# Performance work log

Measured on AMD Instinct MI355X. Metric: run time of the kernel, lower is better.

## Reference

```python
import jax, jax.numpy as jnp
import numpy as np

QBITS = 8  # fake-quant bit width from q_config
DT_RANK = 128
D_STATE = 16


def fake_quant_tensor(x, bits=QBITS):
    """Per-tensor symmetric fake quantization (quantize-dequantize) with STE."""
    qmax = 2.0 ** (bits - 1) - 1.0
    s = jnp.maximum(jnp.max(jnp.abs(x)) / qmax, 1e-8)
    q = jnp.clip(jnp.round(x / s), -qmax - 1.0, qmax) * s
    return x + jax.lax.stop_gradient(q - x)


def fake_quant_per_channel(w, bits=QBITS):
    """Per-output-channel symmetric fake quantization for weights [out, in]."""
    qmax = 2.0 ** (bits - 1) - 1.0
    s = jnp.maximum(jnp.max(jnp.abs(w), axis=-1, keepdims=True) / qmax, 1e-8)
    q = jnp.clip(jnp.round(w / s), -qmax - 1.0, qmax) * s
    return w + jax.lax.stop_gradient(q - w)


def setup_inputs() -> dict:
    key = jax.random.key(0)
    ks = jax.random.split(key, 8)
    B, L, D_MODEL = 2, 4096, 2048
    d_inner = D_MODEL  # expand = 1.0
    x = jax.random.normal(ks[0], (B, L, D_MODEL), jnp.float32)
    prompt = 0.1 * jax.random.normal(ks[1], (B, L, D_STATE), jnp.float32)
    # x_proj: Linear(d_inner -> dt_rank + 2*d_state), no bias
    Wx = jax.random.normal(ks[2], (DT_RANK + 2 * D_STATE, d_inner), jnp.float32) / np.sqrt(d_inner)
    # dt_proj: Linear(dt_rank -> d_inner), with bias
    Wdt = jax.random.normal(ks[3], (d_inner, DT_RANK), jnp.float32) / np.sqrt(DT_RANK)
    bdt = 0.1 * jax.random.normal(ks[4], (d_inner,), jnp.float32)
    # S4D-real init for A_log, D skip param (standard Mamba selective-scan params)
    A_log = jnp.log(jnp.tile(jnp.arange(1, D_STATE + 1, dtype=jnp.float32), (d_inner, 1)))
    Dskip = jax.random.normal(ks[5], (d_inner,), jnp.float32)
    return dict(x=x, prompt=prompt, Wx=Wx, Wdt=Wdt, bdt=bdt, A_log=A_log, Dskip=Dskip)


def reference(x, prompt, Wx, Wdt, bdt, A_log, Dskip):
    # x_proj with fake-quantized weight, then split into dt / B / C
    x_dbl = jnp.einsum('bld,od->blo', x, fake_quant_per_channel(Wx))
    dts = x_dbl[..., :DT_RANK]
    Bs = x_dbl[..., DT_RANK:DT_RANK + D_STATE]
    Cs = x_dbl[..., DT_RANK + D_STATE:]
    # dt_proj with fake-quantized weight
    dts = jnp.einsum('blr,or->blo', dts, fake_quant_per_channel(Wdt)) + bdt
    # activation fake-quant of scan inputs
    u_q = fake_quant_tensor(x)          # [B, L, d_inner]
    dt_q = fake_quant_tensor(dts)       # [B, L, d_inner]
    B_q = fake_quant_tensor(Bs)         # [B, L, d_state]
    C_q = fake_quant_tensor(Cs + prompt)  # [B, L, d_state]
    # selective scan (quantized SSM weights A, D)
    A = -jnp.exp(fake_quant_per_channel(A_log))  # [d_inner, d_state]
    D_q = fake_quant_tensor(Dskip)               # [d_inner]
    dt = jax.nn.softplus(dt_q)

    def step(h, inp):
        u_t, dt_t, B_t, C_t = inp  # [B,d], [B,d], [B,n], [B,n]
        dA = jnp.exp(dt_t[:, :, None] * A)             # [B, d, n]
        dBu = (dt_t * u_t)[:, :, None] * B_t[:, None, :]
        h = dA * h + dBu                               # [B, d, n]
        y = jnp.einsum('bdn,bn->bd', h, C_t)
        return h, y

    Bsz, L, d = x.shape
    h0 = jnp.zeros((Bsz, d, D_STATE), x.dtype)
    xs = (jnp.swapaxes(u_q, 0, 1), jnp.swapaxes(dt, 0, 1),
          jnp.swapaxes(B_q, 0, 1), jnp.swapaxes(C_q, 0, 1))
    _, ys = jax.lax.scan(step, h0, xs)  # ys: [L, B, d]
    return jnp.swapaxes(ys, 0, 1) + u_q * D_q
```

## Files before the change

kernel.cpp:

```cpp
#include <hip/hip_runtime.h>
#include <hip/hip_bf16.h>

#define BSZ    2
#define LSEQ   4096
#define DMODEL 2048
#define DTR    128
#define DST    16
#define ODIM   160
#define MROWS  (BSZ*LSEQ)
#define CH     64
#define TT     (LSEQ/CH)
#define LOG2E  1.44269504088896340736f
#define LN2    0.69314718055994530942f

typedef short  short8  __attribute__((ext_vector_type(8)));
typedef float  floatx4 __attribute__((ext_vector_type(4)));

__device__ __forceinline__ unsigned short f2bf(float f) {
    unsigned u = __float_as_uint(f);
    u += 0x7fffu + ((u >> 16) & 1u);
    return (unsigned short)(u >> 16);
}
__device__ __forceinline__ float quantv(float x, float s, float inv_s) {
    float q = rintf(x * inv_s);
    q = fminf(fmaxf(q, -128.0f), 127.0f);
    return q * s;
}
__device__ __forceinline__ float softplus_fast(float v) {
    float t = __builtin_amdgcn_exp2f(-fabsf(v) * LOG2E);
    return fmaxf(v, 0.0f) + LN2 * __log2f(1.0f + t);
}
__device__ __forceinline__ float scale_from_bits(unsigned bits) {
    return fmaxf(__uint_as_float(bits) * (1.0f/127.0f), 1e-8f);
}
__device__ __forceinline__ int pidx(int r, int k, int K) {
    return (r >> 4)*(16*K) + ((k >> 5) << 9) + (((r & 15) + (((k & 31) >> 3) << 4)) << 3) + (k & 7);
}

#define PB_WX  160
#define PB_WDT 128
#define PB_A   128
#define PB_D   1
#define PREP_BLOCKS (PB_WX + PB_WDT + PB_A + PB_D)

__global__ __launch_bounds__(256) void k_prep(
    const float* __restrict__ Wx, const float* __restrict__ Wdt,
    const float* __restrict__ A_log, const float* __restrict__ Dskip,
    unsigned short* __restrict__ Wxq, unsigned short* __restrict__ Wdtq,
    float* __restrict__ a2, float* __restrict__ Dq)
{
    int bid = blockIdx.x, tid = threadIdx.x;
    __shared__ float red[256];
    if (bid < PB_WX) {
        int o = bid, base = o * DMODEL;
        float m = 0.0f;
        for (int i = tid; i < DMODEL; i += 256) m = fmaxf(m, fabsf(Wx[base+i]));
        red[tid] = m; __syncthreads();
        for (int s2 = 128; s2 > 0; s2 >>= 1) { if (tid < s2) red[tid] = fmaxf(red[tid], red[tid+s2]); __syncthreads(); }
        float s = fmaxf(red[0]*(1.0f/127.0f), 1e-8f), inv = 1.0f/s;
        for (int i = tid; i < DMODEL; i += 256)
            Wxq[pidx(o, i, DMODEL)] = f2bf(quantv(Wx[base+i], s, inv));
    } else if (bid < PB_WX + PB_WDT) {
        int n = (bid - PB_WX)*16 + (tid >> 4);
        int k0 = (tid & 15)*8;
        const float* src = Wdt + (size_t)n*DTR + k0;
        float4 v0 = *reinterpret_cast<const float4*>(src);
        float4 v1 = *reinterpret_cast<const float4*>(src + 4);
        float m = fmaxf(fmaxf(fmaxf(fabsf(v0.x), fabsf(v0.y)), fmaxf(fabsf(v0.z), fabsf(v0.w))),
                        fmaxf(fmaxf(fabsf(v1.x), fabsf(v1.y)), fmaxf(fabsf(v1.z), fabsf(v1.w))));
        for (int off = 1; off < 16; off <<= 1) m = fmaxf(m, __shfl_xor(m, off, 16));
        float s = fmaxf(m*(1.0f/127.0f), 1e-8f), inv = 1.0f/s;
        short8 o8;
        o8[0]=(short)f2bf(quantv(v0.x,s,inv)); o8[1]=(short)f2bf(quantv(v0.y,s,inv));
        o8[2]=(short)f2bf(quantv(v0.z,s,inv)); o8[3]=(short)f2bf(quantv(v0.w,s,inv));
        o8[4]=(short)f2bf(quantv(v1.x,s,inv)); o8[5]=(short)f2bf(quantv(v1.y,s,inv));
        o8[6]=(short)f2bf(quantv(v1.z,s,inv)); o8[7]=(short)f2bf(quantv(v1.w,s,inv));
        *reinterpret_cast<short8*>(Wdtq + pidx(n, k0, DTR)) = o8;
    } else if (bid < PB_WX + PB_WDT + PB_A) {
        int d = (bid - PB_WX - PB_WDT)*16 + (tid >> 4);
        int n = tid & 15;
        float v = A_log[d*DST + n];
        float m = fabsf(v);
        for (int off = 1; off < 16; off <<= 1) m = fmaxf(m, __shfl_xor(m, off, 16));
        float s = fmaxf(m*(1.0f/127.0f), 1e-8f);
        float q = quantv(v, s, 1.0f/s);
        a2[d*DST + n] = -expf(q) * LOG2E;
    } else {
        float m = 0.0f;
        for (int i = tid; i < DMODEL; i += 256) m = fmaxf(m, fabsf(Dskip[i]));
        red[tid] = m; __syncthreads();
        for (int s2 = 128; s2 > 0; s2 >>= 1) { if (tid < s2) red[tid] = fmaxf(red[tid], red[tid+s2]); __syncthreads(); }
        float s = fmaxf(red[0]*(1.0f/127.0f), 1e-8f), inv = 1.0f/s;
        for (int i = tid; i < DMODEL; i += 256) Dq[i] = quantv(Dskip[i], s, inv);
    }
}

__global__ __launch_bounds__(256) void k_mm1(
    const float* __restrict__ x, const unsigned short* __restrict__ Wxq,
    const float* __restrict__ prompt,
    unsigned short* __restrict__ xdblbf, float* __restrict__ xbc,
    unsigned* __restrict__ scales)
{
    int tid = threadIdx.x, w = tid >> 6, lane = tid & 63;
    int mrow = lane & 15, quad = lane >> 4;
    int mt = blockIdx.x, m0 = mt*16, k0 = w*512;
    floatx4 acc[10] = {};
    float xmax = 0.0f;
    const float* arow = x + (size_t)(m0 + mrow)*DMODEL + k0 + quad*8;
    for (int kk = 0; kk < 512; kk += 32) {
        const float4* ap = reinterpret_cast<const float4*>(arow + kk);
        float4 a0 = ap[0], a1 = ap[1];
        xmax = fmaxf(xmax, fmaxf(fmaxf(fabsf(a0.x), fabsf(a0.y)), fmaxf(fabsf(a0.z), fabsf(a0.w))));
        xmax = fmaxf(xmax, fmaxf(fmaxf(fabsf(a1.x), fabsf(a1.y)), fmaxf(fabsf(a1.z), fabsf(a1.w))));
        short8 af;
        af[0]=(short)f2bf(a0.x); af[1]=(short)f2bf(a0.y); af[2]=(short)f2bf(a0.z); af[3]=(short)f2bf(a0.w);
        af[4]=(short)f2bf(a1.x); af[5]=(short)f2bf(a1.y); af[6]=(short)f2bf(a1.z); af[7]=(short)f2bf(a1.w);
        int kcidx = (k0 + kk) >> 5;
        #pragma unroll
        for (int j = 0; j < 10; ++j) {
            short8 bf = *reinterpret_cast<const short8*>(Wxq + j*16*DMODEL + kcidx*512 + lane*8);
            acc[j] = __builtin_amdgcn_mfma_f32_16x16x32_bf16(af, bf, acc[j], 0, 0, 0);
        }
    }
    for (int off = 32; off; off >>= 1) xmax = fmaxf(xmax, __shfl_xor(xmax, off, 64));
    __shared__ float red[4*2560];
    __shared__ float redB[256], redC[256];
    __shared__ float wred[4];
    if (lane == 0) wred[w] = xmax;
    #pragma unroll
    for (int j = 0; j < 10; ++j) {
        float4 v = make_float4(acc[j][0], acc[j][1], acc[j][2], acc[j][3]);
        *reinterpret_cast<float4*>(&red[w*2560 + (j*16 + mrow)*16 + quad*4]) = v;
    }
    __syncthreads();
    float bmax = 0.0f, cmax = 0.0f;
    #pragma unroll
    for (int j = 0; j < 10; ++j) {
        int e = j*256 + tid;
        float v = red[e] + red[2560+e] + red[5120+e] + red[7680+e];
        int col = e >> 4, rowin = e & 15, row = m0 + rowin;
        if (col < DTR) {
            xdblbf[mt*16*DTR + ((col>>5)<<9) + ((rowin + (((col&31)>>3)<<4))<<3) + (col&7)] = f2bf(v);
        } else if (col < DTR + DST) {
            bmax = fmaxf(bmax, fabsf(v));
            xbc[(size_t)row*32 + (col - DTR)] = v;
        } else {
            v += prompt[(size_t)row*DST + (col - DTR - DST)];
            cmax = fmaxf(cmax, fabsf(v));
            xbc[(size_t)row*32 + 16 + (col - DTR - DST)] = v;
        }
    }
    redB[tid] = bmax; redC[tid] = cmax; __syncthreads();
    for (int s2 = 128; s2 > 0; s2 >>= 1) {
        if (tid < s2) { redB[tid] = fmaxf(redB[tid], redB[tid+s2]); redC[tid] = fmaxf(redC[tid], redC[tid+s2]); }
        __syncthreads();
    }
    if (tid == 0) {
        atomicMax(&scales[0], __float_as_uint(fmaxf(fmaxf(wred[0], wred[1]), fmaxf(wred[2], wred[3]))));
        atomicMax(&scales[1], __float_as_uint(redB[0]));
        atomicMax(&scales[2], __float_as_uint(redC[0]));
    }
}

__global__ __launch_bounds__(256) void k_dmaxu(
    const unsigned short* __restrict__ Ap, const unsigned short* __restrict__ Bp,
    const float* __restrict__ bdt, const float* __restrict__ x,
    signed char* __restrict__ u8, unsigned* __restrict__ scales)
{
    int tid = threadIdx.x, w = tid >> 6, lane = tid & 63;
    int mrow = lane & 15;
    int mt = blockIdx.x >> 4, nt = blockIdx.x & 15;
    int mtile = mt*4 + w, n0 = nt*128;
    short8 afr[4];
    const unsigned short* ab = Ap + (size_t)mtile*16*DTR + lane*8;
    #pragma unroll
    for (int kc = 0; kc < 4; ++kc) afr[kc] = *reinterpret_cast<const short8*>(ab + (kc<<9));
    float dmax = 0.0f;
    #pragma unroll
    for (int j = 0; j < 8; ++j) {
        const unsigned short* bb = Bp + (size_t)(n0/16 + j)*16*DTR + lane*8;
        floatx4 acc = {};
        #pragma unroll
        for (int kc = 0; kc < 4; ++kc) {
            short8 bf = *reinterpret_cast<const short8*>(bb + (kc<<9));
            acc = __builtin_amdgcn_mfma_f32_16x16x32_bf16(afr[kc], bf, acc, 0, 0, 0);
        }
        float bv = bdt[n0 + j*16 + mrow];
        #pragma unroll
        for (int r = 0; r < 4; ++r) dmax = fmaxf(dmax, fabsf(acc[r] + bv));
    }
    float s_u = scale_from_bits(scales[0]);
    float inv_su = 1.0f / s_u;
    const float4* xs = reinterpret_cast<const float4*>(x) + (size_t)blockIdx.x*2048;
    unsigned* uo = reinterpret_cast<unsigned*>(u8) + (size_t)blockIdx.x*2048;
    #pragma unroll
    for (int i = 0; i < 8; ++i) {
        float4 v = xs[i*256 + tid];
        int q0 = (int)fminf(fmaxf(rintf(v.x*inv_su), -128.0f), 127.0f);
        int q1 = (int)fminf(fmaxf(rintf(v.y*inv_su), -128.0f), 127.0f);
        int q2 = (int)fminf(fmaxf(rintf(v.z*inv_su), -128.0f), 127.0f);
        int q3 = (int)fminf(fmaxf(rintf(v.w*inv_su), -128.0f), 127.0f);
        uo[i*256 + tid] = (q0 & 255) | ((q1 & 255) << 8) | ((q2 & 255) << 16) | ((unsigned)(q3 & 255) << 24);
    }
    for (int off = 32; off; off >>= 1) dmax = fmaxf(dmax, __shfl_xor(dmax, off, 64));
    __shared__ float wd[4];
    if (lane == 0) wd[w] = dmax;
    __syncthreads();
    if (tid == 0)
        atomicMax(&scales[3], __float_as_uint(fmaxf(fmaxf(wd[0], wd[1]), fmaxf(wd[2], wd[3]))));
}

__global__ __launch_bounds__(256) void k_scan1(
    const unsigned short* __restrict__ Ap, const unsigned short* __restrict__ Bp,
    const float* __restrict__ bdt, const signed char* __restrict__ u8,
    const float* __restrict__ xbc, const float* __restrict__ a2,
    const unsigned* __restrict__ scales,
    float* __restrict__ Aprod, float* __restrict__ hfin)
{
    int bid = blockIdx.x, tid = threadIdx.x;
    int w = tid >> 6, lane = tid & 63;
    int mrow = lane & 15, quad = lane >> 4;
    int b = bid >> 9, rem = bid & 511, dblk = rem >> 6, ch = rem & 63;
    int d0 = dblk*256, t0 = ch*TT;
    int d = d0 + tid;
    float s_u  = scale_from_bits(scales[0]);
    float s_B  = scale_from_bits(scales[1]), inv_sB  = 1.0f/s_B;
    float s_dt = scale_from_bits(scales[3]), inv_sdt = 1.0f/s_dt;
    float a2r[16];
    {
        const float4* ap = reinterpret_cast<const float4*>(a2 + (size_t)d*DST);
        float4 v0 = ap[0], v1 = ap[1], v2 = ap[2], v3 = ap[3];
        a2r[0]=v0.x; a2r[1]=v0.y; a2r[2]=v0.z; a2r[3]=v0.w;
        a2r[4]=v1.x; a2r[5]=v1.y; a2r[6]=v1.z; a2r[7]=v1.w;
        a2r[8]=v2.x; a2r[9]=v2.y; a2r[10]=v2.z; a2r[11]=v2.w;
        a2r[12]=v3.x; a2r[13]=v3.y; a2r[14]=v3.z; a2r[15]=v3.w;
    }
    float h[16];
    #pragma unroll
    for (int n = 0; n < 16; ++n) h[n] = 0.0f;
    float sdt = 0.0f;
    __shared__ float lds_dts[32*256];
    __shared__ unsigned lds_u[32*64];
    __shared__ __align__(16) float Bq_p[32*16];
    for (int st = 0; st < 2; ++st) {
        int tb = t0 + st*32;
        int gm0 = (b*LSEQ + tb) >> 4;
        short8 afr[2][4];
        #pragma unroll
        for (int rt = 0; rt < 2; ++rt)
            #pragma unroll
            for (int kc = 0; kc < 4; ++kc)
                afr[rt][kc] = *reinterpret_cast<const short8*>(Ap + (size_t)(gm0+rt)*16*DTR + (kc<<9) + lane*8);
        #pragma unroll
        for (int j = 0; j < 4; ++j) {
            int ntile = dblk*16 + w*4 + j;
            int dloc = w*64 + j*16 + mrow;
            float bdtv = bdt[d0 + dloc];
            short8 bfr[4];
            #pragma unroll
            for (int kc = 0; kc < 4; ++kc)
                bfr[kc] = *reinterpret_cast<const short8*>(Bp + (size_t)ntile*16*DTR + (kc<<9) + lane*8);
            #pragma unroll
            for (int rt = 0; rt < 2; ++rt) {
                floatx4 acc = {};
                #pragma unroll
                for (int kc = 0; kc < 4; ++kc)
                    acc = __builtin_amdgcn_mfma_f32_16x16x32_bf16(afr[rt][kc], bfr[kc], acc, 0, 0, 0);
                #pragma unroll
                for (int r = 0; r < 4; ++r)
                    lds_dts[(rt*16 + quad*4 + r)*256 + dloc] = acc[r] + bdtv;
            }
        }
        {
            const unsigned* ub = reinterpret_cast<const unsigned*>(u8 + (size_t)(b*LSEQ + tb)*DMODEL + d0);
            #pragma unroll
            for (int i = 0; i < 8; ++i) {
                int q = i*256 + tid;
                lds_u[q] = ub[(q >> 6)*(DMODEL/4) + (q & 63)];
            }
            int e = tid;
            Bq_p[e] = quantv(xbc[(size_t)(b*LSEQ + tb + (e>>4))*32 + (e&15)], s_B, inv_sB);
            e = tid + 256;
            Bq_p[e] = quantv(xbc[(size_t)(b*LSEQ + tb + (e>>4))*32 + (e&15)], s_B, inv_sB);
        }
        __syncthreads();
        const signed char* lub = reinterpret_cast<const signed char*>(lds_u);
        for (int t = 0; t < 32; ++t) {
            float dtq = quantv(lds_dts[t*256 + tid], s_dt, inv_sdt);
            float dtv = softplus_fast(dtq);
            float uq  = s_u * (float)lub[t*256 + tid];
            float dtu = dtv * uq;
            sdt += dtv;
            const float4* bq4 = reinterpret_cast<const float4*>(&Bq_p[t*16]);
            float4 b0 = bq4[0], b1 = bq4[1], b2 = bq4[2], b3 = bq4[3];
            float bq[16] = { b0.x,b0.y,b0.z,b0.w, b1.x,b1.y,b1.z,b1.w,
                             b2.x,b2.y,b2.z,b2.w, b3.x,b3.y,b3.z,b3.w };
            #pragma unroll
            for (int n = 0; n < 16; ++n) {
                float dA = __builtin_amdgcn_exp2f(a2r[n]*dtv);
                h[n] = fmaf(dA, h[n], dtu*bq[n]);
            }
        }
        __syncthreads();
    }
    size_t ob = ((size_t)((b*CH + ch)*DMODEL + d))*DST;
    #pragma unroll
    for (int i = 0; i < 4; ++i) {
        float4 av = make_float4(__builtin_amdgcn_exp2f(a2r[4*i+0]*sdt),
                                __builtin_amdgcn_exp2f(a2r[4*i+1]*sdt),
                                __builtin_amdgcn_exp2f(a2r[4*i+2]*sdt),
                                __builtin_amdgcn_exp2f(a2r[4*i+3]*sdt));
        float4 hv = make_float4(h[4*i+0], h[4*i+1], h[4*i+2], h[4*i+3]);
        *reinterpret_cast<float4*>(Aprod + ob + 4*i) = av;
        *reinterpret_cast<float4*>(hfin  + ob + 4*i) = hv;
    }
}

__global__ __launch_bounds__(256) void k_mid(
    float* __restrict__ Aprod, const float* __restrict__ hfin)
{
    int f = blockIdx.x*256 + threadIdx.x;
    int b = f >> 15, dn = f & 32767;
    size_t base = (size_t)b*CH*32768 + dn;
    float h = 0.0f;
    #pragma unroll 4
    for (int ch = 0; ch < CH; ++ch) {
        size_t o = base + (size_t)ch*32768;
        float a = Aprod[o], hf = hfin[o];
        Aprod[o] = h;
        h = fmaf(a, h, hf);
    }
}

__global__ __launch_bounds__(256) void k_scan3(
    const unsigned short* __restrict__ Ap, const unsigned short* __restrict__ Bp,
    const float* __restrict__ bdt, const signed char* __restrict__ u8,
    const float* __restrict__ xbc, const float* __restrict__ a2,
    const float* __restrict__ Dq, const unsigned* __restrict__ scales,
    const float* __restrict__ hinit, float* __restrict__ out)
{
    int bid = blockIdx.x, tid = threadIdx.x;
    int w = tid >> 6, lane = tid & 63;
    int mrow = lane & 15, quad = lane >> 4;
    int b = bid >> 9, rem = bid & 511, dblk = rem >> 6, ch = rem & 63;
    int d0 = dblk*256, t0 = ch*TT;
    int d = d0 + tid;
    float s_u  = scale_from_bits(scales[0]);
    float s_B  = scale_from_bits(scales[1]), inv_sB  = 1.0f/s_B;
    float s_C  = scale_from_bits(scales[2]), inv_sC  = 1.0f/s_C;
    float s_dt = scale_from_bits(scales[3]), inv_sdt = 1.0f/s_dt;
    float dqd = Dq[d];
    float a2r[16];
    {
        const float4* ap = reinterpret_cast<const float4*>(a2 + (size_t)d*DST);
        float4 v0 = ap[0], v1 = ap[1], v2 = ap[2], v3 = ap[3];
        a2r[0]=v0.x; a2r[1]=v0.y; a2r[2]=v0.z; a2r[3]=v0.w;
        a2r[4]=v1.x; a2r[5]=v1.y; a2r[6]=v1.z; a2r[7]=v1.w;
        a2r[8]=v2.x; a2r[9]=v2.y; a2r[10]=v2.z; a2r[11]=v2.w;
        a2r[12]=v3.x; a2r[13]=v3.y; a2r[14]=v3.z; a2r[15]=v3.w;
    }
    size_t ob = ((size_t)((b*CH + ch)*DMODEL + d))*DST;
    float h[16];
    #pragma unroll
    for (int i = 0; i < 4; ++i) {
        float4 hv = *reinterpret_cast<const float4*>(hinit + ob + 4*i);
        h[4*i+0]=hv.x; h[4*i+1]=hv.y; h[4*i+2]=hv.z; h[4*i+3]=hv.w;
    }
    __shared__ float lds_dts[32*256];
    __shared__ unsigned lds_u[32*64];
    __shared__ __align__(16) float Bq_p[32*16];
    __shared__ __align__(16) float Cq_p[32*16];
    for (int st = 0; st < 2; ++st) {
        int tb = t0 + st*32;
        int gm0 = (b*LSEQ + tb) >> 4;
        short8 afr[2][4];
        #pragma unroll
        for (int rt = 0; rt < 2; ++rt)
            #pragma unroll
            for (int kc = 0; kc < 4; ++kc)
                afr[rt][kc] = *reinterpret_cast<const short8*>(Ap + (size_t)(gm0+rt)*16*DTR + (kc<<9) + lane*8);
        #pragma unroll
        for (int j = 0; j < 4; ++j) {
            int ntile = dblk*16 + w*4 + j;
            int dloc = w*64 + j*16 + mrow;
            float bdtv = bdt[d0 + dloc];
            short8 bfr[4];
            #pragma unroll
            for (int kc = 0; kc < 4; ++kc)
                bfr[kc] = *reinterpret_cast<const short8*>(Bp + (size_t)ntile*16*DTR + (kc<<9) + lane*8);
            #pragma unroll
            for (int rt = 0; rt < 2; ++rt) {
                floatx4 acc = {};
                #pragma unroll
                for (int kc = 0; kc < 4; ++kc)
                    acc = __builtin_amdgcn_mfma_f32_16x16x32_bf16(afr[rt][kc], bfr[kc], acc, 0, 0, 0);
                #pragma unroll
                for (int r = 0; r < 4; ++r)
                    lds_dts[(rt*16 + quad*4 + r)*256 + dloc] = acc[r] + bdtv;
            }
        }
        {
            const unsigned* ub = reinterpret_cast<const unsigned*>(u8 + (size_t)(b*LSEQ + tb)*DMODEL + d0);
            #pragma unroll
            for (int i = 0; i < 8; ++i) {
                int q = i*256 + tid;
                lds_u[q] = ub[(q >> 6)*(DMODEL/4) + (q & 63)];
            }
            int e = tid;
            size_t px = (size_t)(b*LSEQ + tb + (e>>4))*32;
            Bq_p[e] = quantv(xbc[px + (e&15)],      s_B, inv_sB);
            Cq_p[e] = quantv(xbc[px + 16 + (e&15)], s_C, inv_sC);
            e = tid + 256;
            px = (size_t)(b*LSEQ + tb + (e>>4))*32;
            Bq_p[e] = quantv(xbc[px + (e&15)],      s_B, inv_sB);
            Cq_p[e] = quantv(xbc[px + 16 + (e&15)], s_C, inv_sC);
        }
        __syncthreads();
        const signed char* lub = reinterpret_cast<const signed char*>(lds_u);
        for (int t = 0; t < 32; ++t) {
            float dtq = quantv(lds_dts[t*256 + tid], s_dt, inv_sdt);
            float dtv = softplus_fast(dtq);
            float uq  = s_u * (float)lub[t*256 + tid];
            float dtu = dtv * uq;
            const float4* bq4 = reinterpret_cast<const float4*>(&Bq_p[t*16]);
            const float4* cq4 = reinterpret_cast<const float4*>(&Cq_p[t*16]);
            float4 b0 = bq4[0], b1 = bq4[1], b2 = bq4[2], b3 = bq4[3];
            float4 c0 = cq4[0], c1 = cq4[1], c2 = cq4[2], c3 = cq4[3];
            float bq[16] = { b0.x,b0.y,b0.z,b0.w, b1.x,b1.y,b1.z,b1.w,
                             b2.x,b2.y,b2.z,b2.w, b3.x,b3.y,b3.z,b3.w };
            float cq[16] = { c0.x,c0.y,c0.z,c0.w, c1.x,c1.y,c1.z,c1.w,
                             c2.x,c2.y,c2.z,c2.w, c3.x,c3.y,c3.z,c3.w };
            float y = 0.0f;
            #pragma unroll
            for (int n = 0; n < 16; ++n) {
                float dA = __builtin_amdgcn_exp2f(a2r[n]*dtv);
                h[n] = fmaf(dA, h[n], dtu*bq[n]);
                y = fmaf(h[n], cq[n], y);
            }
            __builtin_nontemporal_store(y + uq * dqd, out + (size_t)(b*LSEQ + tb + t)*DMODEL + d);
        }
        __syncthreads();
    }
}

extern "C" void kernel_launch(void* const* d_in, const int* in_sizes, int n_in,
                              void* d_out, int out_size, void* d_ws, size_t ws_size,
                              hipStream_t stream)
{
    const float* x      = (const float*)d_in[0];
    const float* prompt = (const float*)d_in[1];
    const float* Wx     = (const float*)d_in[2];
    const float* Wdt    = (const float*)d_in[3];
    const float* bdt    = (const float*)d_in[4];
    const float* A_log  = (const float*)d_in[5];
    const float* Dskip  = (const float*)d_in[6];
    float* out = (float*)d_out;
    char* ws = (char*)d_ws;
    size_t off = 0;
    unsigned* scales       = (unsigned*)(ws + off);        off += 256;
    unsigned short* Wxq    = (unsigned short*)(ws + off);  off += (size_t)ODIM*DMODEL*2;
    unsigned short* Wdtq   = (unsigned short*)(ws + off);  off += (size_t)DMODEL*DTR*2;
    float* a2              = (float*)(ws + off);           off += (size_t)DMODEL*DST*4;
    float* Dq              = (float*)(ws + off);           off += (size_t)DMODEL*4;
    float* xbc             = (float*)(ws + off);           off += (size_t)MROWS*32*4;
    unsigned short* xdblbf = (unsigned short*)(ws + off);  off += (size_t)MROWS*DTR*2;
    signed char* u8        = (signed char*)(ws + off);     off += (size_t)MROWS*DMODEL;
    float* Aprod           = (float*)(ws + off);           off += (size_t)BSZ*CH*DMODEL*DST*4;
    float* hfin            = (float*)(ws + off);           off += (size_t)BSZ*CH*DMODEL*DST*4;

    hipMemsetAsync(scales, 0, 256, stream);
    hipLaunchKernelGGL(k_prep, dim3(PREP_BLOCKS), dim3(256), 0, stream,
                       Wx, Wdt, A_log, Dskip, Wxq, Wdtq, a2, Dq);
    hipLaunchKernelGGL(k_mm1, dim3(MROWS/16), dim3(256), 0, stream,
                       x, Wxq, prompt, xdblbf, xbc, scales);
    hipLaunchKernelGGL(k_dmaxu, dim3((MROWS/64)*(DMODEL/128)), dim3(256), 0, stream,
                       xdblbf, Wdtq, bdt, x, u8, scales);
    hipLaunchKernelGGL(k_scan1, dim3(BSZ*8*CH), dim3(256), 0, stream,
                       xdblbf, Wdtq, bdt, u8, xbc, a2, scales, Aprod, hfin);
    hipLaunchKernelGGL(k_mid, dim3(BSZ*DMODEL*DST/256), dim3(256), 0, stream,
                       Aprod, hfin);
    hipLaunchKernelGGL(k_scan3, dim3(BSZ*8*CH), dim3(256), 0, stream,
                       xdblbf, Wdtq, bdt, u8, xbc, a2, Dq, scales, Aprod, out);
}
```

Baseline: 309.7 us.

## Fuse dt-max into x_proj kernel and u quantization into scan1, drop k_dmaxu

The dt_proj max-reduction moves into k_mm1, which now multiplies its 16-row tile by all of Wdt from LDS. The x-to-int8 quantization moves into k_scan1, which writes u8 for k_scan3. This removes a kernel launch and one pass that re-read x and the bf16 dt tiles. The scan kernels now stage 16 timesteps instead of 32, with a padded LDS stride, and pack the state update into two-wide float vectors that may map to packed FP32 instructions. In exchange, k_mm1 does much more MFMA and Wdt-load work per block, and the scan loops have more staging and barrier rounds.

```diff
diff --git a/kernel.cpp b/kernel.cpp
--- a/kernel.cpp
+++ b/kernel.cpp
@@ -10,11 +10,13 @@
 #define MROWS  (BSZ*LSEQ)
 #define CH     64
 #define TT     (LSEQ/CH)
+#define STRD   258
 #define LOG2E  1.44269504088896340736f
 #define LN2    0.69314718055994530942f
 
 typedef short  short8  __attribute__((ext_vector_type(8)));
 typedef float  floatx4 __attribute__((ext_vector_type(4)));
+typedef float  floatx2 __attribute__((ext_vector_type(2)));
 
 __device__ __forceinline__ unsigned short f2bf(float f) {
     unsigned u = __float_as_uint(f);
@@ -97,6 +99,7 @@
 
 __global__ __launch_bounds__(256) void k_mm1(
     const float* __restrict__ x, const unsigned short* __restrict__ Wxq,
+    const unsigned short* __restrict__ Wdtq, const float* __restrict__ bdt,
     const float* __restrict__ prompt,
     unsigned short* __restrict__ xdblbf, float* __restrict__ xbc,
     unsigned* __restrict__ scales)
@@ -125,7 +128,8 @@
     for (int off = 32; off; off >>= 1) xmax = fmaxf(xmax, __shfl_xor(xmax, off, 64));
     __shared__ float red[4*2560];
     __shared__ float redB[256], redC[256];
-    __shared__ float wred[4];
+    __shared__ float wred[4], wd[4];
+    __shared__ unsigned short lds_abf[2048];
     if (lane == 0) wred[w] = xmax;
     #pragma unroll
     for (int j = 0; j < 10; ++j) {
@@ -140,7 +144,10 @@
         float v = red[e] + red[2560+e] + red[5120+e] + red[7680+e];
         int col = e >> 4, rowin = e & 15, row = m0 + rowin;
         if (col < DTR) {
-            xdblbf[mt*16*DTR + ((col>>5)<<9) + ((rowin + (((col&31)>>3)<<4))<<3) + (col&7)] = f2bf(v);
+            int off = ((col>>5)<<9) + ((rowin + (((col&31)>>3)<<4))<<3) + (col&7);
+            unsigned short bfb = f2bf(v);
+            xdblbf[mt*16*DTR + off] = bfb;
+            lds_abf[off] = bfb;
         } else if (col < DTR + DST) {
             bmax = fmaxf(bmax, fabsf(v));
             xbc[(size_t)row*32 + (col - DTR)] = v;
@@ -155,66 +162,40 @@
         if (tid < s2) { redB[tid] = fmaxf(redB[tid], redB[tid+s2]); redC[tid] = fmaxf(redC[tid], redC[tid+s2]); }
         __syncthreads();
     }
+    short8 afr[4];
+    #pragma unroll
+    for (int kc = 0; kc < 4; ++kc)
+        afr[kc] = *reinterpret_cast<const short8*>(lds_abf + (kc<<9) + lane*8);
+    float dmax = 0.0f;
+    for (int jj = 0; jj < 32; ++jj) {
+        int ntile = w*32 + jj;
+        const unsigned short* bb = Wdtq + (size_t)ntile*16*DTR + lane*8;
+        floatx4 acc2 = {};
+        #pragma unroll
+        for (int kc = 0; kc < 4; ++kc) {
+            short8 bf = *reinterpret_cast<const short8*>(bb + (kc<<9));
+            acc2 = __builtin_amdgcn_mfma_f32_16x16x32_bf16(afr[kc], bf, acc2, 0, 0, 0);
+        }
+        float bv = bdt[ntile*16 + mrow];
+        #pragma unroll
+        for (int r = 0; r < 4; ++r) dmax = fmaxf(dmax, fabsf(acc2[r] + bv));
+    }
+    for (int off = 32; off; off >>= 1) dmax = fmaxf(dmax, __shfl_xor(dmax, off, 64));
+    if (lane == 0) wd[w] = dmax;
+    __syncthreads();
     if (tid == 0) {
         atomicMax(&scales[0], __float_as_uint(fmaxf(fmaxf(wred[0], wred[1]), fmaxf(wred[2], wred[3]))));
         atomicMax(&scales[1], __float_as_uint(redB[0]));
         atomicMax(&scales[2], __float_as_uint(redC[0]));
-    }
-}
-
-__global__ __launch_bounds__(256) void k_dmaxu(
+        atomicMax(&scales[3], __float_as_uint(fmaxf(fmaxf(wd[0], wd[1]), fmaxf(wd[2], wd[3]))));
+    }
+}
+
+__global__ __launch_bounds__(256) void k_scan1(
     const unsigned short* __restrict__ Ap, const unsigned short* __restrict__ Bp,
     const float* __restrict__ bdt, const float* __restrict__ x,
-    signed char* __restrict__ u8, unsigned* __restrict__ scales)
-{
-    int tid = threadIdx.x, w = tid >> 6, lane = tid & 63;
-    int mrow = lane & 15;
-    int mt = blockIdx.x >> 4, nt = blockIdx.x & 15;
-    int mtile = mt*4 + w, n0 = nt*128;
-    short8 afr[4];
-    const unsigned short* ab = Ap + (size_t)mtile*16*DTR + lane*8;
-    #pragma unroll
-    for (int kc = 0; kc < 4; ++kc) afr[kc] = *reinterpret_cast<const short8*>(ab + (kc<<9));
-    float dmax = 0.0f;
-    #pragma unroll
-    for (int j = 0; j < 8; ++j) {
-        const unsigned short* bb = Bp + (size_t)(n0/16 + j)*16*DTR + lane*8;
-        floatx4 acc = {};
-        #pragma unroll
-        for (int kc = 0; kc < 4; ++kc) {
-            short8 bf = *reinterpret_cast<const short8*>(bb + (kc<<9));
-            acc = __builtin_amdgcn_mfma_f32_16x16x32_bf16(afr[kc], bf, acc, 0, 0, 0);
-        }
-        float bv = bdt[n0 + j*16 + mrow];
-        #pragma unroll
-        for (int r = 0; r < 4; ++r) dmax = fmaxf(dmax, fabsf(acc[r] + bv));
-    }
-    float s_u = scale_from_bits(scales[0]);
-    float inv_su = 1.0f / s_u;
-    const float4* xs = reinterpret_cast<const float4*>(x) + (size_t)blockIdx.x*2048;
-    unsigned* uo = reinterpret_cast<unsigned*>(u8) + (size_t)blockIdx.x*2048;
-    #pragma unroll
-    for (int i = 0; i < 8; ++i) {
-        float4 v = xs[i*256 + tid];
-        int q0 = (int)fminf(fmaxf(rintf(v.x*inv_su), -128.0f), 127.0f);
-        int q1 = (int)fminf(fmaxf(rintf(v.y*inv_su), -128.0f), 127.0f);
-        int q2 = (int)fminf(fmaxf(rintf(v.z*inv_su), -128.0f), 127.0f);
-        int q3 = (int)fminf(fmaxf(rintf(v.w*inv_su), -128.0f), 127.0f);
-        uo[i*256 + tid] = (q0 & 255) | ((q1 & 255) << 8) | ((q2 & 255) << 16) | ((unsigned)(q3 & 255) << 24);
-    }
-    for (int off = 32; off; off >>= 1) dmax = fmaxf(dmax, __shfl_xor(dmax, off, 64));
-    __shared__ float wd[4];
-    if (lane == 0) wd[w] = dmax;
-    __syncthreads();
-    if (tid == 0)
-        atomicMax(&scales[3], __float_as_uint(fmaxf(fmaxf(wd[0], wd[1]), fmaxf(wd[2], wd[3]))));
-}
-
-__global__ __launch_bounds__(256) void k_scan1(
-    const unsigned short* __restrict__ Ap, const unsigned short* __restrict__ Bp,
-    const float* __restrict__ bdt, const signed char* __restrict__ u8,
     const float* __restrict__ xbc, const float* __restrict__ a2,
-    const unsigned* __restrict__ scales,
+    const unsigned* __restrict__ scales, unsigned* __restrict__ u8g,
     float* __restrict__ Aprod, float* __restrict__ hfin)
 {
     int bid = blockIdx.x, tid = threadIdx.x;
@@ -223,94 +204,88 @@
     int b = bid >> 9, rem = bid & 511, dblk = rem >> 6, ch = rem & 63;
     int d0 = dblk*256, t0 = ch*TT;
     int d = d0 + tid;
-    float s_u  = scale_from_bits(scales[0]);
+    float s_u  = scale_from_bits(scales[0]), inv_su = 1.0f/s_u;
     float s_B  = scale_from_bits(scales[1]), inv_sB  = 1.0f/s_B;
     float s_dt = scale_from_bits(scales[3]), inv_sdt = 1.0f/s_dt;
-    float a2r[16];
+    floatx2 a22[8];
     {
-        const float4* ap = reinterpret_cast<const float4*>(a2 + (size_t)d*DST);
-        float4 v0 = ap[0], v1 = ap[1], v2 = ap[2], v3 = ap[3];
-        a2r[0]=v0.x; a2r[1]=v0.y; a2r[2]=v0.z; a2r[3]=v0.w;
-        a2r[4]=v1.x; a2r[5]=v1.y; a2r[6]=v1.z; a2r[7]=v1.w;
-        a2r[8]=v2.x; a2r[9]=v2.y; a2r[10]=v2.z; a2r[11]=v2.w;
-        a2r[12]=v3.x; a2r[13]=v3.y; a2r[14]=v3.z; a2r[15]=v3.w;
-    }
-    float h[16];
-    #pragma unroll
-    for (int n = 0; n < 16; ++n) h[n] = 0.0f;
+        const floatx2* ap = reinterpret_cast<const floatx2*>(a2 + (size_t)d*DST);
+        #pragma unroll
+        for (int i = 0; i < 8; ++i) a22[i] = ap[i];
+    }
+    floatx2 h2[8];
+    #pragma unroll
+    for (int i = 0; i < 8; ++i) h2[i] = (floatx2){0.0f, 0.0f};
     float sdt = 0.0f;
-    __shared__ float lds_dts[32*256];
-    __shared__ unsigned lds_u[32*64];
-    __shared__ __align__(16) float Bq_p[32*16];
-    for (int st = 0; st < 2; ++st) {
-        int tb = t0 + st*32;
-        int gm0 = (b*LSEQ + tb) >> 4;
-        short8 afr[2][4];
-        #pragma unroll
-        for (int rt = 0; rt < 2; ++rt)
-            #pragma unroll
-            for (int kc = 0; kc < 4; ++kc)
-                afr[rt][kc] = *reinterpret_cast<const short8*>(Ap + (size_t)(gm0+rt)*16*DTR + (kc<<9) + lane*8);
+    __shared__ float lds_dts[16*STRD];
+    __shared__ unsigned lds_u[16*64];
+    __shared__ __align__(16) float Bq_p[16*16];
+    for (int st = 0; st < TT/16; ++st) {
+        int tb = t0 + st*16;
+        int gm = (b*LSEQ + tb) >> 4;
+        short8 afr[4];
+        #pragma unroll
+        for (int kc = 0; kc < 4; ++kc)
+            afr[kc] = *reinterpret_cast<const short8*>(Ap + (size_t)gm*16*DTR + (kc<<9) + lane*8);
         #pragma unroll
         for (int j = 0; j < 4; ++j) {
             int ntile = dblk*16 + w*4 + j;
             int dloc = w*64 + j*16 + mrow;
             float bdtv = bdt[d0 + dloc];
-            short8 bfr[4];
-            #pragma unroll
-            for (int kc = 0; kc < 4; ++kc)
-                bfr[kc] = *reinterpret_cast<const short8*>(Bp + (size_t)ntile*16*DTR + (kc<<9) + lane*8);
-            #pragma unroll
-            for (int rt = 0; rt < 2; ++rt) {
-                floatx4 acc = {};
-                #pragma unroll
-                for (int kc = 0; kc < 4; ++kc)
-                    acc = __builtin_amdgcn_mfma_f32_16x16x32_bf16(afr[rt][kc], bfr[kc], acc, 0, 0, 0);
-                #pragma unroll
-                for (int r = 0; r < 4; ++r)
-                    lds_dts[(rt*16 + quad*4 + r)*256 + dloc] = acc[r] + bdtv;
-            }
+            floatx4 acc = {};
+            #pragma unroll
+            for (int kc = 0; kc < 4; ++kc) {
+                short8 bf = *reinterpret_cast<const short8*>(Bp + (size_t)ntile*16*DTR + (kc<<9) + lane*8);
+                acc = __builtin_amdgcn_mfma_f32_16x16x32_bf16(afr[kc], bf, acc, 0, 0, 0);
+            }
+            #pragma unroll
+            for (int r = 0; r < 4; ++r)
+                lds_dts[(quad*4 + r)*STRD + dloc] = acc[r] + bdtv;
         }
         {
-            const unsigned* ub = reinterpret_cast<const unsigned*>(u8 + (size_t)(b*LSEQ + tb)*DMODEL + d0);
-            #pragma unroll
-            for (int i = 0; i < 8; ++i) {
-                int q = i*256 + tid;
-                lds_u[q] = ub[(q >> 6)*(DMODEL/4) + (q & 63)];
-            }
-            int e = tid;
-            Bq_p[e] = quantv(xbc[(size_t)(b*LSEQ + tb + (e>>4))*32 + (e&15)], s_B, inv_sB);
-            e = tid + 256;
-            Bq_p[e] = quantv(xbc[(size_t)(b*LSEQ + tb + (e>>4))*32 + (e&15)], s_B, inv_sB);
+            const float4* x4 = reinterpret_cast<const float4*>(x);
+            #pragma unroll
+            for (int i = 0; i < 4; ++i) {
+                int q = i*256 + tid, row = q >> 6, c4 = q & 63;
+                size_t gi = (size_t)(b*LSEQ + tb + row)*(DMODEL/4) + dblk*64 + c4;
+                float4 v = x4[gi];
+                int q0 = (int)fminf(fmaxf(rintf(v.x*inv_su), -128.0f), 127.0f);
+                int q1 = (int)fminf(fmaxf(rintf(v.y*inv_su), -128.0f), 127.0f);
+                int q2 = (int)fminf(fmaxf(rintf(v.z*inv_su), -128.0f), 127.0f);
+                int q3 = (int)fminf(fmaxf(rintf(v.w*inv_su), -128.0f), 127.0f);
+                unsigned u = (q0 & 255) | ((q1 & 255) << 8) | ((q2 & 255) << 16) | ((unsigned)(q3 & 255) << 24);
+                lds_u[row*64 + c4] = u;
+                u8g[gi] = u;
+            }
+            Bq_p[tid] = quantv(xbc[(size_t)(b*LSEQ + tb + (tid>>4))*32 + (tid&15)], s_B, inv_sB);
         }
         __syncthreads();
         const signed char* lub = reinterpret_cast<const signed char*>(lds_u);
-        for (int t = 0; t < 32; ++t) {
-            float dtq = quantv(lds_dts[t*256 + tid], s_dt, inv_sdt);
+        for (int t = 0; t < 16; ++t) {
+            float dtq = quantv(lds_dts[t*STRD + tid], s_dt, inv_sdt);
             float dtv = softplus_fast(dtq);
             float uq  = s_u * (float)lub[t*256 + tid];
             float dtu = dtv * uq;
             sdt += dtv;
-            const float4* bq4 = reinterpret_cast<const float4*>(&Bq_p[t*16]);
-            float4 b0 = bq4[0], b1 = bq4[1], b2 = bq4[2], b3 = bq4[3];
-            float bq[16] = { b0.x,b0.y,b0.z,b0.w, b1.x,b1.y,b1.z,b1.w,
-                             b2.x,b2.y,b2.z,b2.w, b3.x,b3.y,b3.z,b3.w };
-            #pragma unroll
-            for (int n = 0; n < 16; ++n) {
-                float dA = __builtin_amdgcn_exp2f(a2r[n]*dtv);
-                h[n] = fmaf(dA, h[n], dtu*bq[n]);
+            floatx2 dtv2 = {dtv, dtv}, dtu2 = {dtu, dtu};
+            const floatx2* bq2 = reinterpret_cast<const floatx2*>(&Bq_p[t*16]);
+            #pragma unroll
+            for (int n2 = 0; n2 < 8; ++n2) {
+                floatx2 e = a22[n2] * dtv2;
+                floatx2 dA; dA.x = __builtin_amdgcn_exp2f(e.x); dA.y = __builtin_amdgcn_exp2f(e.y);
+                h2[n2] = dA*h2[n2] + bq2[n2]*dtu2;
             }
         }
         __syncthreads();
     }
     size_t ob = ((size_t)((b*CH + ch)*DMODEL + d))*DST;
+    floatx2 sdt2 = {sdt, sdt};
     #pragma unroll
     for (int i = 0; i < 4; ++i) {
-        float4 av = make_float4(__builtin_amdgcn_exp2f(a2r[4*i+0]*sdt),
-                                __builtin_amdgcn_exp2f(a2r[4*i+1]*sdt),
-                                __builtin_amdgcn_exp2f(a2r[4*i+2]*sdt),
-                                __builtin_amdgcn_exp2f(a2r[4*i+3]*sdt));
-        float4 hv = make_float4(h[4*i+0], h[4*i+1], h[4*i+2], h[4*i+3]);
+        floatx2 e0 = a22[2*i] * sdt2, e1 = a22[2*i+1] * sdt2;
+        float4 av = make_float4(__builtin_amdgcn_exp2f(e0.x), __builtin_amdgcn_exp2f(e0.y),
+                                __builtin_amdgcn_exp2f(e1.x), __builtin_amdgcn_exp2f(e1.y));
+        float4 hv = make_float4(h2[2*i].x, h2[2*i].y, h2[2*i+1].x, h2[2*i+1].y);
         *reinterpret_cast<float4*>(Aprod + ob + 4*i) = av;
         *reinterpret_cast<float4*>(hfin  + ob + 4*i) = hv;
     }
@@ -334,7 +309,7 @@
 
 __global__ __launch_bounds__(256) void k_scan3(
     const unsigned short* __restrict__ Ap, const unsigned short* __restrict__ Bp,
-    const float* __restrict__ bdt, const signed char* __restrict__ u8,
+    const float* __restrict__ bdt, const unsigned* __restrict__ u8g,
     const float* __restrict__ xbc, const float* __restrict__ a2,
     const float* __restrict__ Dq, const unsigned* __restrict__ scales,
     const float* __restrict__ hinit, float* __restrict__ out)
@@ -350,93 +325,76 @@
     float s_C  = scale_from_bits(scales[2]), inv_sC  = 1.0f/s_C;
     float s_dt = scale_from_bits(scales[3]), inv_sdt = 1.0f/s_dt;
     float dqd = Dq[d];
-    float a2r[16];
+    floatx2 a22[8];
     {
-        const float4* ap = reinterpret_cast<const float4*>(a2 + (size_t)d*DST);
-        float4 v0 = ap[0], v1 = ap[1], v2 = ap[2], v3 = ap[3];
-        a2r[0]=v0.x; a2r[1]=v0.y; a2r[2]=v0.z; a2r[3]=v0.w;
-        a2r[4]=v1.x; a2r[5]=v1.y; a2r[6]=v1.z; a2r[7]=v1.w;
-        a2r[8]=v2.x; a2r[9]=v2.y; a2r[10]=v2.z; a2r[11]=v2.w;
-        a2r[12]=v3.x; a2r[13]=v3.y; a2r[14]=v3.z; a2r[15]=v3.w;
+        const floatx2* ap = reinterpret_cast<const floatx2*>(a2 + (size_t)d*DST);
+        #pragma unroll
+        for (int i = 0; i < 8; ++i) a22[i] = ap[i];
     }
     size_t ob = ((size_t)((b*CH + ch)*DMODEL + d))*DST;
-    float h[16];
+    floatx2 h2[8];
     #pragma unroll
     for (int i = 0; i < 4; ++i) {
         float4 hv = *reinterpret_cast<const float4*>(hinit + ob + 4*i);
-        h[4*i+0]=hv.x; h[4*i+1]=hv.y; h[4*i+2]=hv.z; h[4*i+3]=hv.w;
-    }
-    __shared__ float lds_dts[32*256];
-    __shared__ unsigned lds_u[32*64];
-    __shared__ __align__(16) float Bq_p[32*16];
-    __shared__ __align__(16) float Cq_p[32*16];
-    for (int st = 0; st < 2; ++st) {
-        int tb = t0 + st*32;
-        int gm0 = (b*LSEQ + tb) >> 4;
-        short8 afr[2][4];
-        #pragma unroll
-        for (int rt = 0; rt < 2; ++rt)
-            #pragma unroll
-            for (int kc = 0; kc < 4; ++kc)
-                afr[rt][kc] = *reinterpret_cast<const short8*>(Ap + (size_t)(gm0+rt)*16*DTR + (kc<<9) + lane*8);
+        h2[2*i]   = (floatx2){hv.x, hv.y};
+        h2[2*i+1] = (floatx2){hv.z, hv.w};
+    }
+    __shared__ float lds_dts[16*STRD];
+    __shared__ unsigned lds_u[16*64];
+    __shared__ __align__(16) float Bq_p[16*16];
+    __shared__ __align__(16) float Cq_p[16*16];
+    for (int st = 0; st < TT/16; ++st) {
+        int tb = t0 + st*16;
+        int gm = (b*LSEQ + tb) >> 4;
+        short8 afr[4];
+        #pragma unroll
+        for (int kc = 0; kc < 4; ++kc)
+            afr[kc] = *reinterpret_cast<const short8*>(Ap + (size_t)gm*16*DTR + (kc<<9) + lane*8);
         #pragma unroll
         for (int j = 0; j < 4; ++j) {
             int ntile = dblk*16 + w*4 + j;
             int dloc = w*64 + j*16 + mrow;
             float bdtv = bdt[d0 + dloc];
-            short8 bfr[4];
-            #pragma unroll
-            for (int kc = 0; kc < 4; ++kc)
-                bfr[kc] = *reinterpret_cast<const short8*>(Bp + (size_t)ntile*16*DTR + (kc<<9) + lane*8);
-            #pragma unroll
-            for (int rt = 0; rt < 2; ++rt) {
-                floatx4 acc = {};
-                #pragma unroll
-                for (int kc = 0; kc < 4; ++kc)
-                    acc = __builtin_amdgcn_mfma_f32_16x16x32_bf16(afr[rt][kc], bfr[kc], acc, 0, 0, 0);
-                #pragma unroll
-                for (int r = 0; r < 4; ++r)
-                    lds_dts[(rt*16 + quad*4 + r)*256 + dloc] = acc[r] + bdtv;
-            }
+            floatx4 acc = {};
+            #pragma unroll
+            for (int kc = 0; kc < 4; ++kc) {
+                short8 bf = *reinterpret_cast<const short8*>(Bp + (size_t)ntile*16*DTR + (kc<<9) + lane*8);
+                acc = __builtin_amdgcn_mfma_f32_16x16x32_bf16(afr[kc], bf, acc, 0, 0, 0);
+            }
+            #pragma unroll
+            for (int r = 0; r < 4; ++r)
+                lds_dts[(quad*4 + r)*STRD + dloc] = acc[r] + bdtv;
         }
         {
-            const unsigned* ub = reinterpret_cast<const unsigned*>(u8 + (size_t)(b*LSEQ + tb)*DMODEL + d0);
-            #pragma unroll
-            for (int i = 0; i < 8; ++i) {
-                int q = i*256 + tid;
-                lds_u[q] = ub[(q >> 6)*(DMODEL/4) + (q & 63)];
-            }
-            int e = tid;
-            size_t px = (size_t)(b*LSEQ + tb + (e>>4))*32;
-            Bq_p[e] = quantv(xbc[px + (e&15)],      s_B, inv_sB);
-            Cq_p[e] = quantv(xbc[px + 16 + (e&15)], s_C, inv_sC);
-            e = tid + 256;
-            px = (size_t)(b*LSEQ + tb + (e>>4))*32;
-            Bq_p[e] = quantv(xbc[px + (e&15)],      s_B, inv_sB);
-            Cq_p[e] = quantv(xbc[px + 16 + (e&15)], s_C, inv_sC);
+            #pragma unroll
+            for (int i = 0; i < 4; ++i) {
+                int q = i*256 + tid, row = q >> 6, c4 = q & 63;
+                size_t gi = (size_t)(b*LSEQ + tb + row)*(DMODEL/4) + dblk*64 + c4;
+                lds_u[row*64 + c4] = u8g[gi];
+            }
+            size_t px = (size_t)(b*LSEQ + tb + (tid>>4))*32;
+            Bq_p[tid] = quantv(xbc[px + (tid&15)],      s_B, inv_sB);
+            Cq_p[tid] = quantv(xbc[px + 16 + (tid&15)], s_C, inv_sC);
         }
         __syncthreads();
         const signed char* lub = reinterpret_cast<const signed char*>(lds_u);
-        for (int t = 0; t < 32; ++t) {
-            float dtq = quantv(lds_dts[t*256 + tid], s_dt, inv_sdt);
+        for (int t = 0; t < 16; ++t) {
+            float dtq = quantv(lds_dts[t*STRD + tid], s_dt, inv_sdt);
             float dtv = softplus_fast(dtq);
             float uq  = s_u * (float)lub[t*256 + tid];
             float dtu = dtv * uq;
-            const float4* bq4 = reinterpret_cast<const float4*>(&Bq_p[t*16]);
-            const float4* cq4 = reinterpret_cast<const float4*>(&Cq_p[t*16]);
-            float4 b0 = bq4[0], b1 = bq4[1], b2 = bq4[2], b3 = bq4[3];
-            float4 c0 = cq4[0], c1 = cq4[1], c2 = cq4[2], c3 = cq4[3];
-            float bq[16] = { b0.x,b0.y,b0.z,b0.w, b1.x,b1.y,b1.z,b1.w,
-                             b2.x,b2.y,b2.z,b2.w, b3.x,b3.y,b3.z,b3.w };
-            float cq[16] = { c0.x,c0.y,c0.z,c0.w, c1.x,c1.y,c1.z,c1.w,
-                             c2.x,c2.y,c2.z,c2.w, c3.x,c3.y,c3.z,c3.w };
-            float y = 0.0f;
-            #pragma unroll
-            for (int n = 0; n < 16; ++n) {
-                float dA = __builtin_amdgcn_exp2f(a2r[n]*dtv);
-                h[n] = fmaf(dA, h[n], dtu*bq[n]);
-                y = fmaf(h[n], cq[n], y);
-            }
+            floatx2 dtv2 = {dtv, dtv}, dtu2 = {dtu, dtu};
+            const floatx2* bq2 = reinterpret_cast<const floatx2*>(&Bq_p[t*16]);
+            const floatx2* cq2 = reinterpret_cast<const floatx2*>(&Cq_p[t*16]);
+            floatx2 y2 = {0.0f, 0.0f};
+            #pragma unroll
+            for (int n2 = 0; n2 < 8; ++n2) {
+                floatx2 e = a22[n2] * dtv2;
+                floatx2 dA; dA.x = __builtin_amdgcn_exp2f(e.x); dA.y = __builtin_amdgcn_exp2f(e.y);
+                h2[n2] = dA*h2[n2] + bq2[n2]*dtu2;
+                y2 = y2 + h2[n2]*cq2[n2];
+            }
+            float y = y2.x + y2.y;
             __builtin_nontemporal_store(y + uq * dqd, out + (size_t)(b*LSEQ + tb + t)*DMODEL + d);
         }
         __syncthreads();
@@ -464,7 +422,7 @@
     float* Dq              = (float*)(ws + off);           off += (size_t)DMODEL*4;
     float* xbc             = (float*)(ws + off);           off += (size_t)MROWS*32*4;
     unsigned short* xdblbf = (unsigned short*)(ws + off);  off += (size_t)MROWS*DTR*2;
-    signed char* u8        = (signed char*)(ws + off);     off += (size_t)MROWS*DMODEL;
+    unsigned* u8g          = (unsigned*)(ws + off);        off += (size_t)MROWS*DMODEL;
     float* Aprod           = (float*)(ws + off);           off += (size_t)BSZ*CH*DMODEL*DST*4;
     float* hfin            = (float*)(ws + off);           off += (size_t)BSZ*CH*DMODEL*DST*4;
 
@@ -472,13 +430,11 @@
     hipLaunchKernelGGL(k_prep, dim3(PREP_BLOCKS), dim3(256), 0, stream,
                        Wx, Wdt, A_log, Dskip, Wxq, Wdtq, a2, Dq);
     hipLaunchKernelGGL(k_mm1, dim3(MROWS/16), dim3(256), 0, stream,
-                       x, Wxq, prompt, xdblbf, xbc, scales);
-    hipLaunchKernelGGL(k_dmaxu, dim3((MROWS/64)*(DMODEL/128)), dim3(256), 0, stream,
-                       xdblbf, Wdtq, bdt, x, u8, scales);
+                       x, Wxq, Wdtq, bdt, prompt, xdblbf, xbc, scales);
     hipLaunchKernelGGL(k_scan1, dim3(BSZ*8*CH), dim3(256), 0, stream,
-                       xdblbf, Wdtq, bdt, u8, xbc, a2, scales, Aprod, hfin);
+                       xdblbf, Wdtq, bdt, x, xbc, a2, scales, u8g, Aprod, hfin);
     hipLaunchKernelGGL(k_mid, dim3(BSZ*DMODEL*DST/256), dim3(256), 0, stream,
                        Aprod, hfin);
     hipLaunchKernelGGL(k_scan3, dim3(BSZ*8*CH), dim3(256), 0, stream,
-                       xdblbf, Wdtq, bdt, u8, xbc, a2, Dq, scales, Aprod, out);
-}
+                       xdblbf, Wdtq, bdt, u8g, xbc, a2, Dq, scales, Aprod, out);
+}
```

Result: slower. 328.3 us (+6.0%).
